# Optimization experiments

Hardware: AMD Instinct MI355X
Metric: run time of the kernel (lower is better)

## Reference

```python
import jax, jax.numpy as jnp
import numpy as np

N_NODES = 100000


def graph_conv(x, edge_index, w_rel, w_root, b):
    # PyG GraphConv with aggr='add':
    # out_i = W_root @ x_i + W_rel @ (sum_{j in N(i)} x_j) + b
    src, dst = edge_index[0], edge_index[1]
    agg = jax.ops.segment_sum(x[src], dst, num_segments=x.shape[0])  # [N, F_in]
    return x @ w_root.T + agg @ w_rel.T + b


def setup_inputs() -> dict:
    key = jax.random.key(0)
    k = jax.random.split(key, 8)
    c_in, c_hid, c_out = 128, 64, 16
    x = jax.random.normal(k[0], (N_NODES, c_in), dtype=jnp.float32)
    edge_index = jax.random.randint(k[1], (2, 640000), 0, N_NODES, dtype=jnp.int64)
    s1 = 1.0 / np.sqrt(c_in)
    s2 = 1.0 / np.sqrt(c_hid)
    return {
        "x": x,
        "edge_index": edge_index,
        "w1_rel": jax.random.uniform(k[2], (c_hid, c_in), jnp.float32, -s1, s1),
        "w1_root": jax.random.uniform(k[3], (c_hid, c_in), jnp.float32, -s1, s1),
        "b1": jax.random.uniform(k[4], (c_hid,), jnp.float32, -s1, s1),
        "w2_rel": jax.random.uniform(k[5], (c_out, c_hid), jnp.float32, -s2, s2),
        "w2_root": jax.random.uniform(k[6], (c_out, c_hid), jnp.float32, -s2, s2),
        "b2": jax.random.uniform(k[7], (c_out,), jnp.float32, -s2, s2),
    }


def reference(x, edge_index, w1_rel, w1_root, b1, w2_rel, w2_root, b2):
    h = graph_conv(x, edge_index, w1_rel, w1_root, b1)
    h = jax.nn.relu(h)
    # dropout is identity in eval mode (deterministic reference)
    h = graph_conv(h, edge_index, w2_rel, w2_root, b2)
    return jax.nn.log_softmax(h, axis=1)
```

## Files before the change

kernel.cpp:

```cpp
#include <hip/hip_runtime.h>
#include <math.h>

constexpr int CIN = 128, CHID = 64, COUT = 16;

__global__ void detect_kernel(const int* __restrict__ e, int* __restrict__ flag) {
    int v = e[2 * threadIdx.x + 1];
    unsigned long long b = __ballot(v == 0);
    if (threadIdx.x == 0) flag[0] = (b == 0xFFFFFFFFFFFFFFFFULL) ? 1 : 0;
}

__global__ void convert_hist(const int* __restrict__ e, int E,
                             const int* __restrict__ flag,
                             int* __restrict__ srcI, int* __restrict__ dstI,
                             int* __restrict__ counts) {
    int is64 = flag[0];
    int stride = gridDim.x * blockDim.x;
    for (int t = blockIdx.x * blockDim.x + threadIdx.x; t < E; t += stride) {
        int s, d;
        if (is64) { s = e[2 * t]; d = e[2 * (E + t)]; }
        else      { s = e[t];     d = e[E + t];       }
        srcI[t] = s;
        dstI[t] = d;
        atomicAdd(&counts[d], 1);
    }
}

__global__ __launch_bounds__(256)
void scan_partials(const int* __restrict__ counts, int N, int* __restrict__ blocksum) {
    __shared__ int red[256];
    const int tid = threadIdx.x;
    const int base = blockIdx.x * 1024 + tid * 4;
    int s = 0;
#pragma unroll
    for (int i = 0; i < 4; ++i) {
        int idx = base + i;
        if (idx < N) s += counts[idx];
    }
    red[tid] = s;
    __syncthreads();
    for (int d = 128; d > 0; d >>= 1) {
        if (tid < d) red[tid] += red[tid + d];
        __syncthreads();
    }
    if (tid == 0) blocksum[blockIdx.x] = red[0];
}

__global__ __launch_bounds__(1024)
void scan_blocksums(const int* __restrict__ blocksum, int NB, int* __restrict__ blockoff) {
    __shared__ int part[1024];
    const int tid = threadIdx.x;
    part[tid] = (tid < NB) ? blocksum[tid] : 0;
    __syncthreads();
    for (int d = 1; d < 1024; d <<= 1) {
        int v = (tid >= d) ? part[tid - d] : 0;
        __syncthreads();
        part[tid] += v;
        __syncthreads();
    }
    if (tid < NB) blockoff[tid] = (tid == 0) ? 0 : part[tid - 1];
}

__global__ __launch_bounds__(256)
void scan_apply(const int* __restrict__ counts, int N, const int* __restrict__ blockoff,
                int* __restrict__ rowptr, int* __restrict__ cursor) {
    __shared__ int part[256];
    const int tid = threadIdx.x;
    const int base = blockIdx.x * 1024 + tid * 4;
    int c[4];
    int s = 0;
#pragma unroll
    for (int i = 0; i < 4; ++i) {
        int idx = base + i;
        c[i] = (idx < N) ? counts[idx] : 0;
        s += c[i];
    }
    part[tid] = s;
    __syncthreads();
    for (int d = 1; d < 256; d <<= 1) {
        int v = (tid >= d) ? part[tid - d] : 0;
        __syncthreads();
        part[tid] += v;
        __syncthreads();
    }
    int prefix = blockoff[blockIdx.x] + ((tid == 0) ? 0 : part[tid - 1]);
#pragma unroll
    for (int i = 0; i < 4; ++i) {
        int idx = base + i;
        if (idx < N) {
            rowptr[idx] = prefix;
            cursor[idx] = prefix;
            prefix += c[i];
            if (idx == N - 1) rowptr[N] = prefix;
        }
    }
}

__global__ void fill_kernel(const int* __restrict__ srcI, const int* __restrict__ dstI,
                            int E, int* __restrict__ cursor, int* __restrict__ edgesrc) {
    int stride = gridDim.x * blockDim.x;
    for (int t = blockIdx.x * blockDim.x + threadIdx.x; t < E; t += stride) {
        int p = atomicAdd(&cursor[dstI[t]], 1);
        edgesrc[p] = srcI[t];
    }
}

template<int K, int OA, int OB, int NSLOT, int T>
__global__ __launch_bounds__(512)
void gemm_dual(const float* __restrict__ X, int N,
               const float* __restrict__ Wa, const float* __restrict__ Wb,
               const float* __restrict__ bias,
               float* __restrict__ Da, float* __restrict__ Db) {
    constexpr int O = OA + OB;
    constexpr int OG = O / 4;
    constexpr int TILE = NSLOT * T;
    constexpr int PADK = K + 4;
    constexpr int BLOCK = OG * NSLOT;
    static_assert(BLOCK == 512, "block size mismatch");

    __shared__ float wT[K * O];
    __shared__ float xs[TILE * PADK];
    const int tid = threadIdx.x;

    for (int i4 = tid; i4 < OA * (K / 4); i4 += BLOCK) {
        int o = i4 % OA, kq = i4 / OA;
        float4 v = *(const float4*)&Wa[o * K + kq * 4];
        wT[(4 * kq + 0) * O + o] = v.x;
        wT[(4 * kq + 1) * O + o] = v.y;
        wT[(4 * kq + 2) * O + o] = v.z;
        wT[(4 * kq + 3) * O + o] = v.w;
    }
    for (int i4 = tid; i4 < OB * (K / 4); i4 += BLOCK) {
        int o = i4 % OB, kq = i4 / OB;
        float4 v = *(const float4*)&Wb[o * K + kq * 4];
        wT[(4 * kq + 0) * O + OA + o] = v.x;
        wT[(4 * kq + 1) * O + OA + o] = v.y;
        wT[(4 * kq + 2) * O + OA + o] = v.z;
        wT[(4 * kq + 3) * O + OA + o] = v.w;
    }

    const int og = tid % OG;
    const int slot = tid / OG;
    const int o4 = og * 4;
    float4 bv = make_float4(0.f, 0.f, 0.f, 0.f);
    if (o4 < OA) bv = *(const float4*)&bias[o4];

    const int n0 = blockIdx.x * TILE;

    for (int i4 = tid; i4 < TILE * (K / 4); i4 += BLOCK) {
        int node = i4 / (K / 4), kq = i4 % (K / 4);
        int n = n0 + node;
        float4 v = make_float4(0.f, 0.f, 0.f, 0.f);
        if (n < N) v = *(const float4*)&X[(size_t)n * K + kq * 4];
        *(float4*)&xs[node * PADK + kq * 4] = v;
    }
    __syncthreads();

    float4 acc[T];
#pragma unroll
    for (int i = 0; i < T; ++i) acc[i] = make_float4(0.f, 0.f, 0.f, 0.f);

    const float* xrow = &xs[slot * T * PADK];
#pragma unroll 4
    for (int k = 0; k < K; ++k) {
        float4 w4 = *(const float4*)&wT[k * O + o4];
#pragma unroll
        for (int i = 0; i < T; ++i) {
            float xv = xrow[i * PADK + k];
            acc[i].x = fmaf(xv, w4.x, acc[i].x);
            acc[i].y = fmaf(xv, w4.y, acc[i].y);
            acc[i].z = fmaf(xv, w4.z, acc[i].z);
            acc[i].w = fmaf(xv, w4.w, acc[i].w);
        }
    }

#pragma unroll
    for (int i = 0; i < T; ++i) {
        int n = n0 + slot * T + i;
        if (n >= N) continue;
        float4 r = acc[i];
        if (o4 < OA) {
            r.x += bv.x; r.y += bv.y; r.z += bv.z; r.w += bv.w;
            *(float4*)&Da[(size_t)n * OA + o4] = r;
        } else {
            *(float4*)&Db[(size_t)n * OB + (o4 - OA)] = r;
        }
    }
}

__global__ void gather_relu64(const int* __restrict__ rowptr, const int* __restrict__ edgesrc,
                              const float* __restrict__ T1, float* __restrict__ A, int N) {
    constexpr int F = 64, Q = F / 4;
    int idx = blockIdx.x * blockDim.x + threadIdx.x;
    int n = idx / Q, q = idx % Q;
    if (n >= N) return;
    int beg = rowptr[n], end = rowptr[n + 1];
    float4 acc = make_float4(0.f, 0.f, 0.f, 0.f);
    for (int j = beg; j < end; ++j) {
        int s = edgesrc[j];
        float4 v = *(const float4*)&T1[(size_t)s * F + q * 4];
        acc.x += v.x; acc.y += v.y; acc.z += v.z; acc.w += v.w;
    }
    float4 a = *(const float4*)&A[(size_t)n * F + q * 4];
    a.x = fmaxf(a.x + acc.x, 0.f);
    a.y = fmaxf(a.y + acc.y, 0.f);
    a.z = fmaxf(a.z + acc.z, 0.f);
    a.w = fmaxf(a.w + acc.w, 0.f);
    *(float4*)&A[(size_t)n * F + q * 4] = a;
}

__global__ void gather_lsm(const int* __restrict__ rowptr, const int* __restrict__ edgesrc,
                           const float* __restrict__ T3, const float* __restrict__ T2,
                           float* __restrict__ out, int N) {
    int idx = blockIdx.x * blockDim.x + threadIdx.x;
    int n = idx / 4, c = idx % 4;
    if (n >= N) return;
    int beg = rowptr[n], end = rowptr[n + 1];
    float4 acc = make_float4(0.f, 0.f, 0.f, 0.f);
    for (int j = beg; j < end; ++j) {
        int s = edgesrc[j];
        float4 v = *(const float4*)&T2[(size_t)s * 16 + c * 4];
        acc.x += v.x; acc.y += v.y; acc.z += v.z; acc.w += v.w;
    }
    float4 t = *(const float4*)&T3[(size_t)n * 16 + c * 4];
    float4 v = make_float4(t.x + acc.x, t.y + acc.y, t.z + acc.z, t.w + acc.w);
    float m = fmaxf(fmaxf(v.x, v.y), fmaxf(v.z, v.w));
    for (int d = 1; d < 4; d <<= 1) m = fmaxf(m, __shfl_xor(m, d, 4));
    float s = expf(v.x - m) + expf(v.y - m) + expf(v.z - m) + expf(v.w - m);
    for (int d = 1; d < 4; d <<= 1) s += __shfl_xor(s, d, 4);
    float ls = m + logf(s);
    float4 r = make_float4(v.x - ls, v.y - ls, v.z - ls, v.w - ls);
    *(float4*)&out[(size_t)n * 16 + c * 4] = r;
}

extern "C" void kernel_launch(void* const* d_in, const int* in_sizes, int n_in,
                              void* d_out, int out_size, void* d_ws, size_t ws_size,
                              hipStream_t stream) {
    const float* X      = (const float*)d_in[0];
    const int*   EIDX   = (const int*)d_in[1];
    const float* W1REL  = (const float*)d_in[2];
    const float* W1ROOT = (const float*)d_in[3];
    const float* B1     = (const float*)d_in[4];
    const float* W2REL  = (const float*)d_in[5];
    const float* W2ROOT = (const float*)d_in[6];
    const float* B2     = (const float*)d_in[7];
    float* OUT = (float*)d_out;

    const int N = in_sizes[0] / CIN;
    const int E = in_sizes[1] / 2;
    const int NB = (N + 1023) / 1024;

    char* wsb = (char*)d_ws;
    size_t off = 0;
    auto alloc = [&](size_t bytes) { void* p = wsb + off; off += (bytes + 255) & ~size_t(255); return p; };

    int* flag     = (int*)alloc(256);
    int* srcI     = (int*)alloc((size_t)E * 4);
    int* dstI     = (int*)alloc((size_t)E * 4);
    int* edgesrc  = (int*)alloc((size_t)E * 4);
    int* counts   = (int*)alloc((size_t)N * 4);
    int* rowptr   = (int*)alloc((size_t)(N + 1) * 4);
    int* cursor   = (int*)alloc((size_t)N * 4);
    int* blocksum = (int*)alloc((size_t)NB * 4);
    int* blockoff = (int*)alloc((size_t)NB * 4);
    float* A      = (float*)alloc((size_t)N * CHID * 4);
    float* Bt     = (float*)alloc((size_t)N * CHID * 4);
    if (off > ws_size) return;

    float* T3 = Bt;
    float* T2 = Bt + (size_t)N * COUT;

    hipMemsetAsync(counts, 0, (size_t)N * 4, stream);

    detect_kernel<<<1, 64, 0, stream>>>(EIDX, flag);
    convert_hist<<<1024, 256, 0, stream>>>(EIDX, E, flag, srcI, dstI, counts);
    scan_partials<<<NB, 256, 0, stream>>>(counts, N, blocksum);
    scan_blocksums<<<1, 1024, 0, stream>>>(blocksum, NB, blockoff);
    scan_apply<<<NB, 256, 0, stream>>>(counts, N, blockoff, rowptr, cursor);
    fill_kernel<<<1024, 256, 0, stream>>>(srcI, dstI, E, cursor, edgesrc);

    {
        constexpr int TILE = 16 * 6;
        int grid = (N + TILE - 1) / TILE;
        gemm_dual<128, 64, 64, 16, 6><<<grid, 512, 0, stream>>>(X, N, W1ROOT, W1REL, B1, A, Bt);
    }

    {
        int threads = N * 16;
        gather_relu64<<<(threads + 255) / 256, 256, 0, stream>>>(rowptr, edgesrc, Bt, A, N);
    }

    {
        constexpr int TILE = 64 * 4;
        int grid = (N + TILE - 1) / TILE;
        gemm_dual<64, 16, 16, 64, 4><<<grid, 512, 0, stream>>>(A, N, W2ROOT, W2REL, B2, T3, T2);
    }

    {
        int threads = N * 4;
        gather_lsm<<<(threads + 255) / 256, 256, 0, stream>>>(rowptr, edgesrc, T3, T2, OUT, N);
    }
}
```

Measured before the change: 223.5 us.

## Tile K dimension in dual GEMM to shrink LDS and raise occupancy

Splits the K reduction of the dual-output GEMM into chunks of 32, staging only a slice of the transposed weights and input tile in shared memory per iteration. Node tile sizes per block are reduced and launch bounds request 6 blocks per CU. The aim is less LDS and fewer registers per block so more waves stay resident and memory latency is hidden. The cost is reloading and transposing the weights once per block per K chunk, plus extra barriers.

```diff
diff --git a/kernel.cpp b/kernel.cpp
--- a/kernel.cpp
+++ b/kernel.cpp
@@ -104,8 +104,8 @@
     }
 }
 
-template<int K, int OA, int OB, int NSLOT, int T>
-__global__ __launch_bounds__(512)
+template<int K, int KT, int OA, int OB, int NSLOT, int T>
+__global__ __launch_bounds__(512, 6)
 void gemm_dual(const float* __restrict__ X, int N,
                const float* __restrict__ Wa, const float* __restrict__ Wb,
                const float* __restrict__ bias,
@@ -113,30 +113,13 @@
     constexpr int O = OA + OB;
     constexpr int OG = O / 4;
     constexpr int TILE = NSLOT * T;
-    constexpr int PADK = K + 4;
+    constexpr int PADKT = KT + 4;
     constexpr int BLOCK = OG * NSLOT;
     static_assert(BLOCK == 512, "block size mismatch");
 
-    __shared__ float wT[K * O];
-    __shared__ float xs[TILE * PADK];
+    __shared__ float wT[KT * O];
+    __shared__ float xs[TILE * PADKT];
     const int tid = threadIdx.x;
-
-    for (int i4 = tid; i4 < OA * (K / 4); i4 += BLOCK) {
-        int o = i4 % OA, kq = i4 / OA;
-        float4 v = *(const float4*)&Wa[o * K + kq * 4];
-        wT[(4 * kq + 0) * O + o] = v.x;
-        wT[(4 * kq + 1) * O + o] = v.y;
-        wT[(4 * kq + 2) * O + o] = v.z;
-        wT[(4 * kq + 3) * O + o] = v.w;
-    }
-    for (int i4 = tid; i4 < OB * (K / 4); i4 += BLOCK) {
-        int o = i4 % OB, kq = i4 / OB;
-        float4 v = *(const float4*)&Wb[o * K + kq * 4];
-        wT[(4 * kq + 0) * O + OA + o] = v.x;
-        wT[(4 * kq + 1) * O + OA + o] = v.y;
-        wT[(4 * kq + 2) * O + OA + o] = v.z;
-        wT[(4 * kq + 3) * O + OA + o] = v.w;
-    }
 
     const int og = tid % OG;
     const int slot = tid / OG;
@@ -146,31 +129,50 @@
 
     const int n0 = blockIdx.x * TILE;
 
-    for (int i4 = tid; i4 < TILE * (K / 4); i4 += BLOCK) {
-        int node = i4 / (K / 4), kq = i4 % (K / 4);
-        int n = n0 + node;
-        float4 v = make_float4(0.f, 0.f, 0.f, 0.f);
-        if (n < N) v = *(const float4*)&X[(size_t)n * K + kq * 4];
-        *(float4*)&xs[node * PADK + kq * 4] = v;
-    }
-    __syncthreads();
-
     float4 acc[T];
 #pragma unroll
     for (int i = 0; i < T; ++i) acc[i] = make_float4(0.f, 0.f, 0.f, 0.f);
 
-    const float* xrow = &xs[slot * T * PADK];
-#pragma unroll 4
-    for (int k = 0; k < K; ++k) {
-        float4 w4 = *(const float4*)&wT[k * O + o4];
-#pragma unroll
-        for (int i = 0; i < T; ++i) {
-            float xv = xrow[i * PADK + k];
-            acc[i].x = fmaf(xv, w4.x, acc[i].x);
-            acc[i].y = fmaf(xv, w4.y, acc[i].y);
-            acc[i].z = fmaf(xv, w4.z, acc[i].z);
-            acc[i].w = fmaf(xv, w4.w, acc[i].w);
-        }
+    for (int kt = 0; kt < K; kt += KT) {
+        for (int i4 = tid; i4 < OA * (KT / 4); i4 += BLOCK) {
+            int o = i4 % OA, kq = i4 / OA;
+            float4 v = *(const float4*)&Wa[o * K + kt + kq * 4];
+            wT[(4 * kq + 0) * O + o] = v.x;
+            wT[(4 * kq + 1) * O + o] = v.y;
+            wT[(4 * kq + 2) * O + o] = v.z;
+            wT[(4 * kq + 3) * O + o] = v.w;
+        }
+        for (int i4 = tid; i4 < OB * (KT / 4); i4 += BLOCK) {
+            int o = i4 % OB, kq = i4 / OB;
+            float4 v = *(const float4*)&Wb[o * K + kt + kq * 4];
+            wT[(4 * kq + 0) * O + OA + o] = v.x;
+            wT[(4 * kq + 1) * O + OA + o] = v.y;
+            wT[(4 * kq + 2) * O + OA + o] = v.z;
+            wT[(4 * kq + 3) * O + OA + o] = v.w;
+        }
+        for (int i4 = tid; i4 < TILE * (KT / 4); i4 += BLOCK) {
+            int node = i4 / (KT / 4), kq = i4 % (KT / 4);
+            int n = n0 + node;
+            float4 v = make_float4(0.f, 0.f, 0.f, 0.f);
+            if (n < N) v = *(const float4*)&X[(size_t)n * K + kt + kq * 4];
+            *(float4*)&xs[node * PADKT + kq * 4] = v;
+        }
+        __syncthreads();
+
+        const float* xrow = &xs[slot * T * PADKT];
+#pragma unroll 8
+        for (int k = 0; k < KT; ++k) {
+            float4 w4 = *(const float4*)&wT[k * O + o4];
+#pragma unroll
+            for (int i = 0; i < T; ++i) {
+                float xv = xrow[i * PADKT + k];
+                acc[i].x = fmaf(xv, w4.x, acc[i].x);
+                acc[i].y = fmaf(xv, w4.y, acc[i].y);
+                acc[i].z = fmaf(xv, w4.z, acc[i].z);
+                acc[i].w = fmaf(xv, w4.w, acc[i].w);
+            }
+        }
+        __syncthreads();
     }
 
 #pragma unroll
@@ -279,9 +281,9 @@
     fill_kernel<<<1024, 256, 0, stream>>>(srcI, dstI, E, cursor, edgesrc);
 
     {
-        constexpr int TILE = 16 * 6;
+        constexpr int TILE = 16 * 4;
         int grid = (N + TILE - 1) / TILE;
-        gemm_dual<128, 64, 64, 16, 6><<<grid, 512, 0, stream>>>(X, N, W1ROOT, W1REL, B1, A, Bt);
+        gemm_dual<128, 32, 64, 64, 16, 4><<<grid, 512, 0, stream>>>(X, N, W1ROOT, W1REL, B1, A, Bt);
     }
 
     {
@@ -290,9 +292,9 @@
     }
 
     {
-        constexpr int TILE = 64 * 4;
+        constexpr int TILE = 64 * 2;
         int grid = (N + TILE - 1) / TILE;
-        gemm_dual<64, 16, 16, 64, 4><<<grid, 512, 0, stream>>>(A, N, W2ROOT, W2REL, B2, T3, T2);
+        gemm_dual<64, 32, 16, 16, 64, 2><<<grid, 512, 0, stream>>>(A, N, W2ROOT, W2REL, B2, T3, T2);
     }
 
     {
```

After: 202.7 us. -9.3%, faster.
